# Kernel optimization log

Hardware: AMD Instinct MI355X
Metric: run time of the kernel (lower is better)

The kernel has to match this reference:

```python
import jax, jax.numpy as jnp
import numpy as np

WS = 4          # window size per axis
HEADS = 3
HEAD_DIM = 32
DIM = 96
DISP = WS // 2  # displacement for shifted windows


def _make_mask(axis):
    # (w^3, w^3) additive mask, -inf across the wrap-around boundary on `axis`
    m = np.zeros((WS, WS, WS, WS, WS, WS), dtype=np.float32)
    d = DISP
    if axis == 0:
        m[-d:, :, :, :-d, :, :] = -np.inf
        m[:-d, :, :, -d:, :, :] = -np.inf
    elif axis == 1:
        m[:, -d:, :, :, :-d, :] = -np.inf
        m[:, :-d, :, :, -d:, :] = -np.inf
    else:
        m[:, :, -d:, :, :, :-d] = -np.inf
        m[:, :, :-d, :, :, -d:] = -np.inf
    return jnp.asarray(m.reshape(WS**3, WS**3))


def setup_inputs() -> dict:
    key = jax.random.key(0)
    k1, k2, k3, k4 = jax.random.split(key, 4)
    inner = HEADS * HEAD_DIM
    x = jax.random.normal(k1, (1, 64, 64, 64, DIM), dtype=jnp.float32)
    w_qkv = jax.random.normal(k2, (3 * inner, DIM), dtype=jnp.float32) * 0.02
    w_out = jax.random.normal(k3, (DIM, inner), dtype=jnp.float32) * 0.02
    b_out = jax.random.normal(k4, (DIM,), dtype=jnp.float32) * 0.02
    return {
        'x': x, 'w_qkv': w_qkv, 'w_out': w_out, 'b_out': b_out,
        'x_mask': _make_mask(0), 'y_mask': _make_mask(1), 'z_mask': _make_mask(2),
    }


def _forward(x, w_qkv, w_out, b_out, x_mask, y_mask, z_mask):
    scale = HEAD_DIM ** -0.5
    b, nx, ny, nz, _ = x.shape
    nwx, nwy, nwz = nx // WS, ny // WS, nz // WS
    seq = WS ** 3
    # cyclic shift by -displacement
    x = jnp.roll(x, shift=(-DISP, -DISP, -DISP), axis=(1, 2, 3))
    qkv = jnp.einsum('bxyzc,oc->bxyzo', x, w_qkv)
    q, k, v = jnp.split(qkv, 3, axis=-1)

    def win(t):  # -> (b, h, n_windows, seq, d)
        t = t.reshape(b, nwx, WS, nwy, WS, nwz, WS, HEADS, HEAD_DIM)
        t = t.transpose(0, 7, 1, 3, 5, 2, 4, 6, 8)
        return t.reshape(b, HEADS, nwx * nwy * nwz, seq, HEAD_DIM)

    q, k, v = win(q), win(k), win(v)
    dots = jnp.einsum('bhwid,bhwjd->bhwij', q, k) * scale

    # shifted-window masking (faithful to original einops relabeling, incl.
    # the final mislabeled rearrange which permutes the window grid)
    d = dots.reshape(b, HEADS, nwx, nwy, nwz, seq, seq)
    d = d.transpose(0, 1, 3, 4, 2, 5, 6)          # (b,h,ny,nz,nx,i,j)
    d = d.at[:, :, :, :, -1].add(x_mask)
    d = d.transpose(0, 1, 4, 3, 2, 5, 6)          # (b,h,nx,nz,ny,i,j)
    d = d.at[:, :, :, :, -1].add(y_mask)
    d = d.transpose(0, 1, 2, 4, 3, 5, 6)          # (b,h,nx,ny,nz,i,j)
    d = d.transpose(0, 1, 4, 2, 3, 5, 6)          # original's final rearrange bug
    dots = d.reshape(b, HEADS, nwx * nwy * nwz, seq, seq)

    attn = jax.nn.softmax(dots, axis=-1)
    out = jnp.einsum('bhwij,bhwjd->bhwid', attn, v)
    # un-window
    out = out.reshape(b, HEADS, nwx, nwy, nwz, WS, WS, WS, HEAD_DIM)
    out = out.transpose(0, 2, 5, 3, 6, 4, 7, 1, 8).reshape(b, nx, ny, nz, HEADS * HEAD_DIM)
    out = jnp.einsum('bxyzc,oc->bxyzo', out, w_out) + b_out
    # cyclic back shift
    return jnp.roll(out, shift=(DISP, DISP, DISP), axis=(1, 2, 3))


def reference(x, w_qkv, w_out, b_out, x_mask, y_mask, z_mask):
    return _forward(x, w_qkv, w_out, b_out, x_mask, y_mask, z_mask)
```

## Files before the change

### kernel.cpp

```cpp
#include <hip/hip_runtime.h>
#include <hip/hip_bf16.h>


using bf4   = __attribute__((ext_vector_type(4))) short;
using bf8   = __attribute__((ext_vector_type(8))) short;
using f32x4 = __attribute__((ext_vector_type(4))) float;

#define SW      104
#define WQ_ROWS 288
#define W_ROWS  384
#define W_SHORTS (W_ROWS * SW)
#define SQK 100
#define SVT  68
#define K_SH (64 * SQK)
#define V_SH (96 * SVT)

__device__ __forceinline__ short f2b(float f) {
  __hip_bfloat16 h = __float2bfloat16(f);
  return *reinterpret_cast<short*>(&h);
}
__device__ __forceinline__ bf4 pk4(const f32x4& a) {
  bf4 s; s[0] = f2b(a[0]); s[1] = f2b(a[1]); s[2] = f2b(a[2]); s[3] = f2b(a[3]);
  return s;
}
__device__ __forceinline__ bf4 pk4s(const f32x4& a, float sc) {
  bf4 s; s[0] = f2b(a[0] * sc); s[1] = f2b(a[1] * sc);
  s[2] = f2b(a[2] * sc); s[3] = f2b(a[3] * sc);
  return s;
}
__device__ __forceinline__ bf8 cvt8(const float4& a, const float4& b) {
  bf8 o;
  o[0] = f2b(a.x); o[1] = f2b(a.y); o[2] = f2b(a.z); o[3] = f2b(a.w);
  o[4] = f2b(b.x); o[5] = f2b(b.y); o[6] = f2b(b.z); o[7] = f2b(b.w);
  return o;
}

#if __has_builtin(__builtin_amdgcn_mfma_f32_16x16x16bf16_1k)
__device__ __forceinline__ f32x4 mfma16(bf4 a, bf4 b, f32x4 c) {
  return __builtin_amdgcn_mfma_f32_16x16x16bf16_1k(a, b, c, 0, 0, 0);
}
#elif __has_builtin(__builtin_amdgcn_mfma_f32_16x16x16_bf16)
__device__ __forceinline__ f32x4 mfma16(bf4 a, bf4 b, f32x4 c) {
  return __builtin_amdgcn_mfma_f32_16x16x16_bf16(a, b, c, 0, 0, 0);
}
#else
__device__ __forceinline__ f32x4 mfma16(bf4 a, bf4 b, f32x4 c) {
  asm("v_mfma_f32_16x16x16_bf16 %0, %1, %2, %0" : "+v"(c) : "v"(a), "v"(b));
  return c;
}
#endif

__global__ void prep_weights(const float* __restrict__ wq, const float* __restrict__ wo,
                             short* __restrict__ wpk) {
  int i = blockIdx.x * 256 + threadIdx.x;
  if (i >= W_SHORTS) return;
  int row = i / SW, c = i - row * SW;
  const float QS = 0.17677669529663687f;
  float v = 0.f;
  if (c < 96) {
    if (row < 96)           v = wq[row * 96 + c] * QS;
    else if (row < WQ_ROWS) v = wq[row * 96 + c];
    else                    v = wo[(row - WQ_ROWS) * 96 + c];
  }
  wpk[i] = f2b(v);
}

__global__ __launch_bounds__(512, 1)
void fused_swin3d(const float* __restrict__ x,
                  const short* __restrict__ wpk,
                  const float* __restrict__ bo,
                  float* __restrict__ out) {
  __shared__ __align__(16) short ls[W_SHORTS + 2 * (K_SH + V_SH)];

  const int tid  = threadIdx.x;
  const int half = tid >> 8;
  short* ls_w  = ls;
  short* ls_k  = ls + W_SHORTS + half * K_SH;
  short* ls_vt = ls + W_SHORTS + 2 * K_SH + half * V_SH;
  const short* ls_wo = ls + WQ_ROWS * SW;

  const int w = (int)blockIdx.x * 2 + half;
  const int p = w >> 8, q = (w >> 4) & 15, r = w & 15;
  const int lane = tid & 63;
  const int wv   = (tid >> 6) & 3;
  const int lr   = lane & 15;
  const int kg   = lane >> 4;
  const int site = wv * 16 + lr;
  const int sy = (lr >> 2) & 3, sz = lr & 3;
  const int ch0 = kg * 8;

  const int gx1 = (q * 4 + wv + 2) & 63, gy1 = (r * 4 + sy + 2) & 63, gz1 = (p * 4 + sz + 2) & 63;
  const int gx2 = (p * 4 + wv + 2) & 63, gy2 = (q * 4 + sy + 2) & 63, gz2 = (r * 4 + sz + 2) & 63;
  const size_t b1 = (size_t)((gx1 * 64 + gy1) * 64 + gz1) * 96;
  const size_t b2 = (size_t)((gx2 * 64 + gy2) * 64 + gz2) * 96;

  float4 xa[6], xb[6];
  #pragma unroll
  for (int f = 0; f < 3; ++f) {
    xa[f]     = *reinterpret_cast<const float4*>(&x[b1 + f * 32 + ch0]);
    xa[3 + f] = *reinterpret_cast<const float4*>(&x[b1 + f * 32 + ch0 + 4]);
  }
  #pragma unroll
  for (int f = 0; f < 3; ++f) {
    xb[f]     = *reinterpret_cast<const float4*>(&x[b2 + f * 32 + ch0]);
    xb[3 + f] = *reinterpret_cast<const float4*>(&x[b2 + f * 32 + ch0 + 4]);
  }
  const float4* wsrc = reinterpret_cast<const float4*>(wpk);
  #pragma unroll
  for (int i = 0; i < 10; ++i) {
    int c = i * 512 + tid;
    if (c < W_SHORTS / 8)
      *reinterpret_cast<float4*>(&ls_w[c * 8]) = wsrc[c];
  }
  bf8 x1[3];
  #pragma unroll
  for (int f = 0; f < 3; ++f) x1[f] = cvt8(xa[f], xa[3 + f]);
  __syncthreads();

  bf4 qn[6];
  #pragma unroll
  for (int n = 0; n < 12; ++n) {
    f32x4 acc = {0.f, 0.f, 0.f, 0.f};
    const short* wrow = &ls_w[(n * 16 + lr) * SW + ch0];
    acc = __builtin_amdgcn_mfma_f32_16x16x32_bf16(*reinterpret_cast<const bf8*>(wrow +  0), x1[0], acc, 0, 0, 0);
    acc = __builtin_amdgcn_mfma_f32_16x16x32_bf16(*reinterpret_cast<const bf8*>(wrow + 32), x1[1], acc, 0, 0, 0);
    acc = __builtin_amdgcn_mfma_f32_16x16x32_bf16(*reinterpret_cast<const bf8*>(wrow + 64), x1[2], acc, 0, 0, 0);
    if (n < 6) qn[n] = pk4(acc);
    else *reinterpret_cast<bf4*>(&ls_k[site * SQK + (n - 6) * 16 + kg * 4]) = pk4(acc);
  }

  bf8 x2[3];
  #pragma unroll
  for (int f = 0; f < 3; ++f) x2[f] = cvt8(xb[f], xb[3 + f]);
  #pragma unroll
  for (int n = 0; n < 6; ++n) {
    f32x4 acc = {0.f, 0.f, 0.f, 0.f};
    const short* wrow = &ls_w[(192 + n * 16 + lr) * SW + ch0];
    acc = __builtin_amdgcn_mfma_f32_16x16x32_bf16(x2[0], *reinterpret_cast<const bf8*>(wrow +  0), acc, 0, 0, 0);
    acc = __builtin_amdgcn_mfma_f32_16x16x32_bf16(x2[1], *reinterpret_cast<const bf8*>(wrow + 32), acc, 0, 0, 0);
    acc = __builtin_amdgcn_mfma_f32_16x16x32_bf16(x2[2], *reinterpret_cast<const bf8*>(wrow + 64), acc, 0, 0, 0);
    *reinterpret_cast<bf4*>(&ls_vt[(n * 16 + lr) * SVT + wv * 16 + kg * 4]) = pk4(acc);
  }
  __syncthreads();

  const bool mx = (q == 15), my = (r == 15);
  const bool killy = my && ((lr >= 8) != (kg >= 2));

  f32x4 osw[3][2];
  #pragma unroll
  for (int h = 0; h < 3; ++h)
    #pragma unroll
    for (int n = 0; n < 2; ++n) osw[h][n] = (f32x4){0.f, 0.f, 0.f, 0.f};

  #pragma unroll
  for (int h = 0; h < 3; ++h) {
    f32x4 sv[4];
    #pragma unroll
    for (int nj = 0; nj < 4; ++nj) {
      const int krow = (nj * 16 + lr) * SQK + h * 32 + kg * 4;
      bf4 ka0 = *reinterpret_cast<const bf4*>(&ls_k[krow]);
      bf4 ka1 = *reinterpret_cast<const bf4*>(&ls_k[krow + 16]);
      f32x4 z = {0.f, 0.f, 0.f, 0.f};
      z = mfma16(ka0, qn[2 * h + 0], z);
      sv[nj] = mfma16(ka1, qn[2 * h + 1], z);
    }
    float sum = 0.f;
    #pragma unroll
    for (int nj = 0; nj < 4; ++nj) {
      const bool kill = killy || (mx && ((wv >= 2) != (nj >= 2)));
      #pragma unroll
      for (int t = 0; t < 4; ++t) {
        float ev = kill ? 0.f : __expf(sv[nj][t]);
        sv[nj][t] = ev;
        sum += ev;
      }
    }
    sum += __shfl_xor(sum, 16);
    sum += __shfl_xor(sum, 32);
    const float inv = 1.f / sum;
    bf4 pb[4];
    #pragma unroll
    for (int t = 0; t < 4; ++t) pb[t] = pk4s(sv[t], inv);
    #pragma unroll
    for (int nc = 0; nc < 2; ++nc) {
      const int vrow = (h * 32 + nc * 16 + lr) * SVT + kg * 4;
      #pragma unroll
      for (int t = 0; t < 4; ++t) {
        bf4 va = *reinterpret_cast<const bf4*>(&ls_vt[vrow + t * 16]);
        osw[h][nc] = mfma16(va, pb[t], osw[h][nc]);
      }
    }
  }

  bf4 ob[6];
  #pragma unroll
  for (int h = 0; h < 3; ++h)
    #pragma unroll
    for (int n = 0; n < 2; ++n) ob[2 * h + n] = pk4(osw[h][n]);

  #pragma unroll
  for (int no = 0; no < 6; ++no) {
    f32x4 acc = {0.f, 0.f, 0.f, 0.f};
    const short* wr = &ls_wo[(no * 16 + lr) * SW + kg * 4];
    #pragma unroll
    for (int c = 0; c < 6; ++c) {
      bf4 wa = *reinterpret_cast<const bf4*>(wr + c * 16);
      acc = mfma16(wa, ob[c], acc);
    }
    const float4 bb = *reinterpret_cast<const float4*>(&bo[no * 16 + kg * 4]);
    float4 o4;
    o4.x = acc[0] + bb.x; o4.y = acc[1] + bb.y;
    o4.z = acc[2] + bb.z; o4.w = acc[3] + bb.w;
    *reinterpret_cast<float4*>(&out[b2 + no * 16 + kg * 4]) = o4;
  }
}

extern "C" void kernel_launch(void* const* d_in, const int* in_sizes, int n_in,
                              void* d_out, int out_size, void* d_ws, size_t ws_size,
                              hipStream_t stream) {
  const float* x  = (const float*)d_in[0];
  const float* wq = (const float*)d_in[1];
  const float* wo = (const float*)d_in[2];
  const float* bo = (const float*)d_in[3];

  short* wpk = (short*)d_ws;

  prep_weights<<<(W_SHORTS + 255) / 256, 256, 0, stream>>>(wq, wo, wpk);
  fused_swin3d<<<2048, 512, 0, stream>>>(x, wpk, bo, (float*)d_out);
}
```

Baseline: 100.5 us.

## Process one window per wavefront with register-resident Q/K/V instead of LDS

Each wavefront now handles a whole 64-token window: it computes Q, K and V for all four 16-row chunks in registers and runs attention and the output projection without staging K and V through shared memory or block-wide barriers after the weight load. LDS use drops to the weight tile only, launch bounds allow two blocks per CU, and the grid shrinks to 512 blocks of 8 windows. The cost is heavy register pressure (q/k/v/ob arrays of 4x6 bf4 each), which may cause spills or limit occupancy, and there are fewer blocks to spread across CUs.

```diff
diff --git a/kernel.cpp b/kernel.cpp
--- a/kernel.cpp
+++ b/kernel.cpp
@@ -10,10 +10,6 @@
 #define WQ_ROWS 288
 #define W_ROWS  384
 #define W_SHORTS (W_ROWS * SW)
-#define SQK 100
-#define SVT  68
-#define K_SH (64 * SQK)
-#define V_SH (96 * SVT)
 
 __device__ __forceinline__ short f2b(float f) {
   __hip_bfloat16 h = __float2bfloat16(f);
@@ -65,46 +61,14 @@
   wpk[i] = f2b(v);
 }
 
-__global__ __launch_bounds__(512, 1)
+__global__ __launch_bounds__(512, 2)
 void fused_swin3d(const float* __restrict__ x,
                   const short* __restrict__ wpk,
                   const float* __restrict__ bo,
                   float* __restrict__ out) {
-  __shared__ __align__(16) short ls[W_SHORTS + 2 * (K_SH + V_SH)];
-
-  const int tid  = threadIdx.x;
-  const int half = tid >> 8;
-  short* ls_w  = ls;
-  short* ls_k  = ls + W_SHORTS + half * K_SH;
-  short* ls_vt = ls + W_SHORTS + 2 * K_SH + half * V_SH;
-  const short* ls_wo = ls + WQ_ROWS * SW;
-
-  const int w = (int)blockIdx.x * 2 + half;
-  const int p = w >> 8, q = (w >> 4) & 15, r = w & 15;
-  const int lane = tid & 63;
-  const int wv   = (tid >> 6) & 3;
-  const int lr   = lane & 15;
-  const int kg   = lane >> 4;
-  const int site = wv * 16 + lr;
-  const int sy = (lr >> 2) & 3, sz = lr & 3;
-  const int ch0 = kg * 8;
-
-  const int gx1 = (q * 4 + wv + 2) & 63, gy1 = (r * 4 + sy + 2) & 63, gz1 = (p * 4 + sz + 2) & 63;
-  const int gx2 = (p * 4 + wv + 2) & 63, gy2 = (q * 4 + sy + 2) & 63, gz2 = (r * 4 + sz + 2) & 63;
-  const size_t b1 = (size_t)((gx1 * 64 + gy1) * 64 + gz1) * 96;
-  const size_t b2 = (size_t)((gx2 * 64 + gy2) * 64 + gz2) * 96;
-
-  float4 xa[6], xb[6];
-  #pragma unroll
-  for (int f = 0; f < 3; ++f) {
-    xa[f]     = *reinterpret_cast<const float4*>(&x[b1 + f * 32 + ch0]);
-    xa[3 + f] = *reinterpret_cast<const float4*>(&x[b1 + f * 32 + ch0 + 4]);
-  }
-  #pragma unroll
-  for (int f = 0; f < 3; ++f) {
-    xb[f]     = *reinterpret_cast<const float4*>(&x[b2 + f * 32 + ch0]);
-    xb[3 + f] = *reinterpret_cast<const float4*>(&x[b2 + f * 32 + ch0 + 4]);
-  }
+  __shared__ __align__(16) short ls_w[W_SHORTS];
+
+  const int tid = threadIdx.x;
   const float4* wsrc = reinterpret_cast<const float4*>(wpk);
   #pragma unroll
   for (int i = 0; i < 10; ++i) {
@@ -112,106 +76,129 @@
     if (c < W_SHORTS / 8)
       *reinterpret_cast<float4*>(&ls_w[c * 8]) = wsrc[c];
   }
-  bf8 x1[3];
-  #pragma unroll
-  for (int f = 0; f < 3; ++f) x1[f] = cvt8(xa[f], xa[3 + f]);
+
+  const int w = (int)blockIdx.x * 8 + (tid >> 6);
+  const int p = w >> 8, q = (w >> 4) & 15, r = w & 15;
+  const int lane = tid & 63;
+  const int lr   = lane & 15;
+  const int kg   = lane >> 4;
+  const int sy = (lr >> 2) & 3, sz = lr & 3;
+  const int ch0 = kg * 8;
+  const short* ls_wo = ls_w + WQ_ROWS * SW;
+
   __syncthreads();
 
-  bf4 qn[6];
-  #pragma unroll
-  for (int n = 0; n < 12; ++n) {
-    f32x4 acc = {0.f, 0.f, 0.f, 0.f};
-    const short* wrow = &ls_w[(n * 16 + lr) * SW + ch0];
-    acc = __builtin_amdgcn_mfma_f32_16x16x32_bf16(*reinterpret_cast<const bf8*>(wrow +  0), x1[0], acc, 0, 0, 0);
-    acc = __builtin_amdgcn_mfma_f32_16x16x32_bf16(*reinterpret_cast<const bf8*>(wrow + 32), x1[1], acc, 0, 0, 0);
-    acc = __builtin_amdgcn_mfma_f32_16x16x32_bf16(*reinterpret_cast<const bf8*>(wrow + 64), x1[2], acc, 0, 0, 0);
-    if (n < 6) qn[n] = pk4(acc);
-    else *reinterpret_cast<bf4*>(&ls_k[site * SQK + (n - 6) * 16 + kg * 4]) = pk4(acc);
-  }
-
-  bf8 x2[3];
-  #pragma unroll
-  for (int f = 0; f < 3; ++f) x2[f] = cvt8(xb[f], xb[3 + f]);
-  #pragma unroll
-  for (int n = 0; n < 6; ++n) {
-    f32x4 acc = {0.f, 0.f, 0.f, 0.f};
-    const short* wrow = &ls_w[(192 + n * 16 + lr) * SW + ch0];
-    acc = __builtin_amdgcn_mfma_f32_16x16x32_bf16(x2[0], *reinterpret_cast<const bf8*>(wrow +  0), acc, 0, 0, 0);
-    acc = __builtin_amdgcn_mfma_f32_16x16x32_bf16(x2[1], *reinterpret_cast<const bf8*>(wrow + 32), acc, 0, 0, 0);
-    acc = __builtin_amdgcn_mfma_f32_16x16x32_bf16(x2[2], *reinterpret_cast<const bf8*>(wrow + 64), acc, 0, 0, 0);
-    *reinterpret_cast<bf4*>(&ls_vt[(n * 16 + lr) * SVT + wv * 16 + kg * 4]) = pk4(acc);
-  }
-  __syncthreads();
+  bf4 qn[4][6], kn[4][6], vn[4][6];
+  #pragma unroll
+  for (int sc = 0; sc < 4; ++sc) {
+    const int gx1 = (q * 4 + sc + 2) & 63, gy1 = (r * 4 + sy + 2) & 63, gz1 = (p * 4 + sz + 2) & 63;
+    const int gx2 = (p * 4 + sc + 2) & 63, gy2 = (q * 4 + sy + 2) & 63, gz2 = (r * 4 + sz + 2) & 63;
+    const size_t b1 = (size_t)((gx1 * 64 + gy1) * 64 + gz1) * 96;
+    const size_t b2 = (size_t)((gx2 * 64 + gy2) * 64 + gz2) * 96;
+
+    float4 xa0 = *reinterpret_cast<const float4*>(&x[b1 +  0 + ch0]);
+    float4 xa1 = *reinterpret_cast<const float4*>(&x[b1 + 32 + ch0]);
+    float4 xa2 = *reinterpret_cast<const float4*>(&x[b1 + 64 + ch0]);
+    float4 xa3 = *reinterpret_cast<const float4*>(&x[b1 +  0 + ch0 + 4]);
+    float4 xa4 = *reinterpret_cast<const float4*>(&x[b1 + 32 + ch0 + 4]);
+    float4 xa5 = *reinterpret_cast<const float4*>(&x[b1 + 64 + ch0 + 4]);
+    float4 xb0 = *reinterpret_cast<const float4*>(&x[b2 +  0 + ch0]);
+    float4 xb1 = *reinterpret_cast<const float4*>(&x[b2 + 32 + ch0]);
+    float4 xb2 = *reinterpret_cast<const float4*>(&x[b2 + 64 + ch0]);
+    float4 xb3 = *reinterpret_cast<const float4*>(&x[b2 +  0 + ch0 + 4]);
+    float4 xb4 = *reinterpret_cast<const float4*>(&x[b2 + 32 + ch0 + 4]);
+    float4 xb5 = *reinterpret_cast<const float4*>(&x[b2 + 64 + ch0 + 4]);
+
+    bf8 x1[3], x2[3];
+    x1[0] = cvt8(xa0, xa3); x1[1] = cvt8(xa1, xa4); x1[2] = cvt8(xa2, xa5);
+    x2[0] = cvt8(xb0, xb3); x2[1] = cvt8(xb1, xb4); x2[2] = cvt8(xb2, xb5);
+
+    #pragma unroll
+    for (int n = 0; n < 12; ++n) {
+      f32x4 acc = {0.f, 0.f, 0.f, 0.f};
+      const short* wrow = &ls_w[(n * 16 + lr) * SW + ch0];
+      acc = __builtin_amdgcn_mfma_f32_16x16x32_bf16(*reinterpret_cast<const bf8*>(wrow +  0), x1[0], acc, 0, 0, 0);
+      acc = __builtin_amdgcn_mfma_f32_16x16x32_bf16(*reinterpret_cast<const bf8*>(wrow + 32), x1[1], acc, 0, 0, 0);
+      acc = __builtin_amdgcn_mfma_f32_16x16x32_bf16(*reinterpret_cast<const bf8*>(wrow + 64), x1[2], acc, 0, 0, 0);
+      if (n < 6) qn[sc][n] = pk4(acc);
+      else       kn[sc][n - 6] = pk4(acc);
+    }
+    #pragma unroll
+    for (int n = 0; n < 6; ++n) {
+      f32x4 acc = {0.f, 0.f, 0.f, 0.f};
+      const short* wrow = &ls_w[(192 + n * 16 + lr) * SW + ch0];
+      acc = __builtin_amdgcn_mfma_f32_16x16x32_bf16(x2[0], *reinterpret_cast<const bf8*>(wrow +  0), acc, 0, 0, 0);
+      acc = __builtin_amdgcn_mfma_f32_16x16x32_bf16(x2[1], *reinterpret_cast<const bf8*>(wrow + 32), acc, 0, 0, 0);
+      acc = __builtin_amdgcn_mfma_f32_16x16x32_bf16(x2[2], *reinterpret_cast<const bf8*>(wrow + 64), acc, 0, 0, 0);
+      vn[sc][n] = pk4(acc);
+    }
+  }
 
   const bool mx = (q == 15), my = (r == 15);
   const bool killy = my && ((lr >= 8) != (kg >= 2));
-
-  f32x4 osw[3][2];
-  #pragma unroll
-  for (int h = 0; h < 3; ++h)
-    #pragma unroll
-    for (int n = 0; n < 2; ++n) osw[h][n] = (f32x4){0.f, 0.f, 0.f, 0.f};
-
-  #pragma unroll
-  for (int h = 0; h < 3; ++h) {
-    f32x4 sv[4];
-    #pragma unroll
-    for (int nj = 0; nj < 4; ++nj) {
-      const int krow = (nj * 16 + lr) * SQK + h * 32 + kg * 4;
-      bf4 ka0 = *reinterpret_cast<const bf4*>(&ls_k[krow]);
-      bf4 ka1 = *reinterpret_cast<const bf4*>(&ls_k[krow + 16]);
-      f32x4 z = {0.f, 0.f, 0.f, 0.f};
-      z = mfma16(ka0, qn[2 * h + 0], z);
-      sv[nj] = mfma16(ka1, qn[2 * h + 1], z);
-    }
-    float sum = 0.f;
-    #pragma unroll
-    for (int nj = 0; nj < 4; ++nj) {
-      const bool kill = killy || (mx && ((wv >= 2) != (nj >= 2)));
-      #pragma unroll
-      for (int t = 0; t < 4; ++t) {
-        float ev = kill ? 0.f : __expf(sv[nj][t]);
-        sv[nj][t] = ev;
-        sum += ev;
+  bf4 ob[4][6];
+
+  #pragma unroll
+  for (int qc = 0; qc < 4; ++qc) {
+    f32x4 osw[6];
+    #pragma unroll
+    for (int c = 0; c < 6; ++c) osw[c] = (f32x4){0.f, 0.f, 0.f, 0.f};
+
+    #pragma unroll
+    for (int h = 0; h < 3; ++h) {
+      f32x4 sv[4];
+      #pragma unroll
+      for (int nj = 0; nj < 4; ++nj) {
+        f32x4 z = {0.f, 0.f, 0.f, 0.f};
+        z = mfma16(kn[nj][2 * h + 0], qn[qc][2 * h + 0], z);
+        sv[nj] = mfma16(kn[nj][2 * h + 1], qn[qc][2 * h + 1], z);
       }
-    }
-    sum += __shfl_xor(sum, 16);
-    sum += __shfl_xor(sum, 32);
-    const float inv = 1.f / sum;
-    bf4 pb[4];
-    #pragma unroll
-    for (int t = 0; t < 4; ++t) pb[t] = pk4s(sv[t], inv);
-    #pragma unroll
-    for (int nc = 0; nc < 2; ++nc) {
-      const int vrow = (h * 32 + nc * 16 + lr) * SVT + kg * 4;
-      #pragma unroll
-      for (int t = 0; t < 4; ++t) {
-        bf4 va = *reinterpret_cast<const bf4*>(&ls_vt[vrow + t * 16]);
-        osw[h][nc] = mfma16(va, pb[t], osw[h][nc]);
+      float sum = 0.f;
+      #pragma unroll
+      for (int nj = 0; nj < 4; ++nj) {
+        const bool kill = killy || (mx && ((qc >= 2) != (nj >= 2)));
+        #pragma unroll
+        for (int t = 0; t < 4; ++t) {
+          float ev = kill ? 0.f : __expf(sv[nj][t]);
+          sv[nj][t] = ev;
+          sum += ev;
+        }
       }
-    }
-  }
-
-  bf4 ob[6];
-  #pragma unroll
-  for (int h = 0; h < 3; ++h)
-    #pragma unroll
-    for (int n = 0; n < 2; ++n) ob[2 * h + n] = pk4(osw[h][n]);
+      sum += __shfl_xor(sum, 16);
+      sum += __shfl_xor(sum, 32);
+      const float inv = 1.f / sum;
+      bf4 pb[4];
+      #pragma unroll
+      for (int t = 0; t < 4; ++t) pb[t] = pk4s(sv[t], inv);
+      #pragma unroll
+      for (int nc = 0; nc < 2; ++nc)
+        #pragma unroll
+        for (int t = 0; t < 4; ++t)
+          osw[2 * h + nc] = mfma16(vn[t][2 * h + nc], pb[t], osw[2 * h + nc]);
+    }
+    #pragma unroll
+    for (int c = 0; c < 6; ++c) ob[qc][c] = pk4(osw[c]);
+  }
 
   #pragma unroll
   for (int no = 0; no < 6; ++no) {
-    f32x4 acc = {0.f, 0.f, 0.f, 0.f};
-    const short* wr = &ls_wo[(no * 16 + lr) * SW + kg * 4];
-    #pragma unroll
-    for (int c = 0; c < 6; ++c) {
-      bf4 wa = *reinterpret_cast<const bf4*>(wr + c * 16);
-      acc = mfma16(wa, ob[c], acc);
-    }
+    bf4 wa[6];
+    #pragma unroll
+    for (int c = 0; c < 6; ++c)
+      wa[c] = *reinterpret_cast<const bf4*>(&ls_wo[(no * 16 + lr) * SW + c * 16 + kg * 4]);
     const float4 bb = *reinterpret_cast<const float4*>(&bo[no * 16 + kg * 4]);
-    float4 o4;
-    o4.x = acc[0] + bb.x; o4.y = acc[1] + bb.y;
-    o4.z = acc[2] + bb.z; o4.w = acc[3] + bb.w;
-    *reinterpret_cast<float4*>(&out[b2 + no * 16 + kg * 4]) = o4;
+    #pragma unroll
+    for (int qc = 0; qc < 4; ++qc) {
+      f32x4 acc = {0.f, 0.f, 0.f, 0.f};
+      #pragma unroll
+      for (int c = 0; c < 6; ++c) acc = mfma16(wa[c], ob[qc][c], acc);
+      const int gx2 = (p * 4 + qc + 2) & 63, gy2 = (q * 4 + sy + 2) & 63, gz2 = (r * 4 + sz + 2) & 63;
+      const size_t b2 = (size_t)((gx2 * 64 + gy2) * 64 + gz2) * 96;
+      float4 o4;
+      o4.x = acc[0] + bb.x; o4.y = acc[1] + bb.y;
+      o4.z = acc[2] + bb.z; o4.w = acc[3] + bb.w;
+      *reinterpret_cast<float4*>(&out[b2 + no * 16 + kg * 4]) = o4;
+    }
   }
 }
 
@@ -226,5 +213,5 @@
   short* wpk = (short*)d_ws;
 
   prep_weights<<<(W_SHORTS + 255) / 256, 256, 0, stream>>>(wq, wo, wpk);
-  fused_swin3d<<<2048, 512, 0, stream>>>(x, wpk, bo, (float*)d_out);
-}
+  fused_swin3d<<<512, 512, 0, stream>>>(x, wpk, bo, (float*)d_out);
+}
```

Result: slower. 109.2 us (+8.7%).
